# Kernel tuning notes

Measured on AMD Instinct MI355X. Metric: run time of the kernel, lower is better.

The kernel has to match this reference:

```python
import jax, jax.numpy as jnp
import numpy as np

N_E, N_C, N_DL, N_IT, N_EP, N_HA, N_CA, N_AS = 11964, 188, 100, 7, 100, 10, 10, 7
D = 128
B, S = 256, 400
N_V = N_E + 1      # hypergraph vertices (exercises)
N_HE = N_C + 1     # hyperedges (concepts)
MEMB = 3           # concept memberships per exercise
BN_EPS = 1e-5


def _hg_v2v_mean(X, pair_v, pair_e):
    # HGNN+ smoothing: vertex -> hyperedge (mean) -> vertex (mean)
    ones_e = jnp.ones(pair_e.shape, X.dtype)
    e_deg = jnp.clip(jax.ops.segment_sum(ones_e, pair_e, num_segments=N_HE), 1.0)
    v_deg = jnp.clip(jax.ops.segment_sum(ones_e, pair_v, num_segments=N_V), 1.0)
    E = jax.ops.segment_sum(X[pair_v], pair_e, num_segments=N_HE) / e_deg[:, None]
    return jax.ops.segment_sum(E[pair_e], pair_v, num_segments=N_V) / v_deg[:, None]


def _hgnnp_conv(X, W, b, gamma, beta, mean, var, pair_v, pair_e, is_last):
    X = X @ W + b
    X = (X - mean) * jax.lax.rsqrt(var + BN_EPS) * gamma + beta  # eval-mode BN
    X = _hg_v2v_mean(X, pair_v, pair_e)
    if not is_last:
        X = jax.nn.relu(X)
    return X


def setup_inputs() -> dict:
    key = jax.random.key(0)
    ks = jax.random.split(key, 32)
    inp = {}
    inp['input_e'] = jax.random.randint(ks[0], (B, S), 0, N_V)
    inp['input_ed'] = jax.random.randint(ks[1], (B, S), 0, N_DL + 1)
    inp['input_ep'] = jax.random.randint(ks[2], (B, S), 0, N_EP + 1)
    inp['input_a'] = jax.random.randint(ks[3], (B, S), 0, 2)
    inp['input_as'] = jax.random.randint(ks[4], (B, S), 0, N_AS + 1)
    inp['input_ha'] = jax.random.randint(ks[5], (B, S), 0, N_HA + 1)
    inp['input_ca'] = jax.random.randint(ks[6], (B, S), 0, N_CA + 1)
    inp['input_it'] = jax.random.randint(ks[7], (B, S), 0, N_IT + 1)
    inp['deliver_h'] = jnp.zeros((B, D), jnp.float32)
    # hypergraph incidence (exercise-concept Q-matrix edges)
    rng = np.random.default_rng(0)
    inp['pair_v'] = jnp.asarray(np.repeat(np.arange(N_V), MEMB))
    inp['pair_e'] = jnp.asarray(rng.integers(0, N_HE, size=N_V * MEMB))
    inp['ec_map'] = jax.random.randint(ks[8], (N_V,), 0, N_HE)
    inp['ecd_map'] = jax.random.randint(ks[9], (N_V,), 0, N_DL + 1)
    # embedding tables (xavier-ish scale)
    def emb(k, n):
        return jax.random.normal(k, (n, D), jnp.float32) * 0.05
    inp['e_table'] = emb(ks[10], N_V)
    inp['c_table'] = emb(ks[11], N_HE)
    inp['ed_table'] = emb(ks[12], N_DL + 1)
    inp['cd_table'] = emb(ks[13], N_DL + 1)
    inp['a_table'] = emb(ks[14], 2)
    inp['it_table'] = emb(ks[15], N_IT + 1)
    inp['ep_table'] = emb(ks[16], N_EP + 1)
    inp['ha_table'] = emb(ks[17], N_HA + 1)
    inp['ca_table'] = emb(ks[18], N_CA + 1)
    inp['as_table'] = emb(ks[19], N_AS + 1)
    # HGNNP conv 1 & 2
    def lin(k, din, dout):
        return jax.random.normal(k, (din, dout), jnp.float32) * (1.0 / np.sqrt(din))
    inp['W1'] = lin(ks[20], D, D); inp['b1'] = jnp.zeros((D,), jnp.float32)
    inp['g1'] = jnp.ones((D,), jnp.float32); inp['be1'] = jnp.zeros((D,), jnp.float32)
    inp['m1'] = jnp.zeros((D,), jnp.float32); inp['v1'] = jnp.ones((D,), jnp.float32)
    inp['W2'] = lin(ks[21], D, D); inp['b2'] = jnp.zeros((D,), jnp.float32)
    inp['g2'] = jnp.ones((D,), jnp.float32); inp['be2'] = jnp.zeros((D,), jnp.float32)
    inp['m2'] = jnp.zeros((D,), jnp.float32); inp['v2'] = jnp.ones((D,), jnp.float32)
    # linear_i: (d_e + d_dl + d_ep + d_c + d_dl) -> d_x
    inp['Wi'] = lin(ks[22], 5 * D, D); inp['bi'] = jnp.zeros((D,), jnp.float32)
    # GRU knowledge-state cell: input = concat(x, a_emb) -> 2D, hidden D, 3 gates
    inp['Wg'] = lin(ks[23], 2 * D, 3 * D)
    inp['Ug'] = lin(ks[24], D, 3 * D)
    inp['bg'] = jnp.zeros((3 * D,), jnp.float32)
    # linear_predicting_e: d_x -> 1
    inp['We'] = lin(ks[25], D, 1); inp['beo'] = jnp.zeros((1,), jnp.float32)
    # linear_predicting_s: 4*d -> 1
    inp['Ws'] = lin(ks[26], 4 * D, 1); inp['bs'] = jnp.zeros((1,), jnp.float32)
    return inp


def reference(input_e, input_ed, input_ep, input_a, input_as, input_ha, input_ca, input_it,
              deliver_h, pair_v, pair_e, ec_map, ecd_map,
              e_table, c_table, ed_table, cd_table, a_table, it_table, ep_table,
              ha_table, ca_table, as_table,
              W1, b1, g1, be1, m1, v1, W2, b2, g2, be2, m2, v2,
              Wi, bi, Wg, Ug, bg, We, beo, Ws, bs):
    # 2-layer HGNN+ over the exercise hypergraph
    X = _hgnnp_conv(e_table, W1, b1, g1, be1, m1, v1, pair_v, pair_e, is_last=False)
    X = _hgnnp_conv(X, W2, b2, g2, be2, m2, v2, pair_v, pair_e, is_last=True)
    # embedding gathers  [B,S,D]
    e_emb = X[input_e]
    c_emb = c_table[ec_map[input_e]]
    cd_emb = cd_table[ecd_map[input_e]]
    ed_emb = ed_table[input_ed]
    ep_emb = ep_table[input_ep]
    x = jnp.tanh(jnp.concatenate([e_emb, ed_emb, ep_emb, c_emb, cd_emb], -1) @ Wi + bi)  # [B,S,D]
    a_emb = a_table[input_a]
    xs = jnp.moveaxis(jnp.concatenate([x, a_emb], -1), 1, 0)  # [S,B,2D]
    xp = jnp.moveaxis(x, 1, 0)                                # [S,B,D]

    def step(h, inputs):
        xin, xq = inputs
        y = jax.nn.sigmoid((h * xq) @ We + beo)[..., 0]  # predict from prior knowledge state
        gi = xin @ Wg + bg
        gh = h @ Ug
        iz, ir, inn = jnp.split(gi, 3, -1)
        hz, hr, hn = jnp.split(gh, 3, -1)
        z = jax.nn.sigmoid(iz + hz)
        r = jax.nn.sigmoid(ir + hr)
        n = jnp.tanh(inn + r * hn)
        return (1.0 - z) * n + z * h, y

    _, ys = jax.lax.scan(step, deliver_h, (xs, xp))
    pred_main = jnp.moveaxis(ys, 0, 1)  # [B,S]
    s_in = jnp.concatenate([ha_table[input_ha], ca_table[input_ca],
                            as_table[input_as], it_table[input_it]], -1)
    pred_s = jax.nn.sigmoid(s_in @ Ws + bs)[..., 0]  # [B,S]
    return pred_s, pred_main
```

## Files before the change

kernel.cpp:

```cpp
#include <hip/hip_runtime.h>

#define N_V   11965
#define N_HE  189
#define NPAIR 35895
#define BB    256
#define SS    400
#define DD    128
#define BSR   102400

typedef __bf16 bf16x8 __attribute__((ext_vector_type(8)));
typedef float  f32x4  __attribute__((ext_vector_type(4)));

__device__ __forceinline__ ushort f2bf(float f) {
    unsigned x = __float_as_uint(f);
    return (ushort)((x + 0x7FFFu + ((x >> 16) & 1u)) >> 16);
}
__device__ __forceinline__ float bf2f(ushort u) { return __uint_as_float(((unsigned)u) << 16); }
__device__ __forceinline__ float sigm(float x) { return 1.f / (1.f + __expf(-x)); }
__device__ __forceinline__ float tanh_f(float x) { return 2.f * sigm(2.f * x) - 1.f; }
__device__ __forceinline__ float blo(unsigned u) { return __uint_as_float(u << 16); }
__device__ __forceinline__ float bhi(unsigned u) { return __uint_as_float(u); }

struct P1Args {
    const int* pair_e;
    const float *b1, *g1, *be1, *m1, *v1;
    const float *b2, *g2, *be2, *m2, *v2;
    const float *W1, *W2, *Wi, *Wg, *Ug;
    const float *ed_t, *ep_t, *c_t, *cd_t, *a_t, *bi, *bg;
    const float *ha_t, *ca_t, *as_t, *it_t, *Ws;
    int* e_deg;
    float* aff;
    ushort *W1T, *W2T, *WiTe, *WgT, *UgT;
    float *edW, *epW, *cW, *cdW, *agi, *sd;
};

__global__ __launch_bounds__(384) void p1_kernel(P1Args A) {
    int bid = blockIdx.x, t = threadIdx.x;
    if (bid == 0) {
        if (t < 128) {
            float s = A.g1[t] * rsqrtf(A.v1[t] + 1e-5f);
            A.aff[t] = s;
            A.aff[128 + t] = A.b1[t] * s + A.be1[t] - A.m1[t] * s;
        } else if (t < 256) {
            int d = t - 128;
            float s = A.g2[d] * rsqrtf(A.v2[d] + 1e-5f);
            A.aff[256 + d] = s;
            A.aff[384 + d] = A.b2[d] * s + A.be2[d] - A.m2[d] * s;
        }
        return;
    }
    bid -= 1;
    if (bid < 94) {
        int p = bid * 384 + t;
        if (p < NPAIR) atomicAdd(&A.e_deg[A.pair_e[p]], 1);
        return;
    }
    bid -= 94;
    if (bid < 43) {
        int i = bid * 384 + t;
        if (i < 16384) { int k = i >> 7, n = i & 127; A.W1T[n * 128 + k] = f2bf(A.W1[i]); }
        return;
    }
    bid -= 43;
    if (bid < 43) {
        int i = bid * 384 + t;
        if (i < 16384) { int k = i >> 7, n = i & 127; A.W2T[n * 128 + k] = f2bf(A.W2[i]); }
        return;
    }
    bid -= 43;
    if (bid < 43) {
        int i = bid * 384 + t;
        if (i < 16384) { int k = i >> 7, n = i & 127; A.WiTe[n * 128 + k] = f2bf(A.Wi[i]); }
        return;
    }
    bid -= 43;
    if (bid < 128) {
        int i = bid * 384 + t;
        if (i < 49152) { int k = i / 384, n = i % 384; A.WgT[n * 128 + k] = f2bf(A.Wg[i]); }
        return;
    }
    bid -= 128;
    if (bid < 128) {
        int i = bid * 384 + t;
        if (i < 49152) { int k = i / 384, n = i % 384; A.UgT[n * 128 + k] = f2bf(A.Ug[i]); }
        return;
    }
    bid -= 128;
    if (bid < 101) {
        if (t < 128) {
            float acc = 0.f;
            for (int k = 0; k < 128; ++k)
                acc += A.ed_t[bid * 128 + k] * A.Wi[(128 + k) * 128 + t];
            A.edW[bid * 128 + t] = acc + A.bi[t];
        }
        return;
    }
    bid -= 101;
    if (bid < 101) {
        if (t < 128) {
            float acc = 0.f;
            for (int k = 0; k < 128; ++k)
                acc += A.ep_t[bid * 128 + k] * A.Wi[(256 + k) * 128 + t];
            A.epW[bid * 128 + t] = acc;
        }
        return;
    }
    bid -= 101;
    if (bid < 189) {
        if (t < 128) {
            float acc = 0.f;
            for (int k = 0; k < 128; ++k)
                acc += A.c_t[bid * 128 + k] * A.Wi[(384 + k) * 128 + t];
            A.cW[bid * 128 + t] = acc;
        }
        return;
    }
    bid -= 189;
    if (bid < 101) {
        if (t < 128) {
            float acc = 0.f;
            for (int k = 0; k < 128; ++k)
                acc += A.cd_t[bid * 128 + k] * A.Wi[(512 + k) * 128 + t];
            A.cdW[bid * 128 + t] = acc;
        }
        return;
    }
    bid -= 101;
    if (bid < 2) {
        float acc = 0.f;
        for (int k = 0; k < 128; ++k)
            acc += A.a_t[bid * 128 + k] * A.Wg[(128 + k) * 384 + t];
        A.agi[bid * 384 + t] = acc + A.bg[t];
        return;
    }
    bid -= 2;
    {
        int r = bid;
        const float* tab; int woff, row;
        if (r < 11)      { tab = A.ha_t; row = r;      woff = 0;   }
        else if (r < 22) { tab = A.ca_t; row = r - 11; woff = 128; }
        else if (r < 30) { tab = A.as_t; row = r - 22; woff = 256; }
        else             { tab = A.it_t; row = r - 30; woff = 384; }
        if (t < 64) {
            float p = tab[row * 128 + t] * A.Ws[woff + t]
                    + tab[row * 128 + 64 + t] * A.Ws[woff + 64 + t];
            #pragma unroll
            for (int o = 32; o > 0; o >>= 1) p += __shfl_xor(p, o);
            if (t == 0) A.sd[r] = p;
        }
    }
}

__global__ void cvt_kernel(const float* __restrict__ src, ushort* __restrict__ dst, int n) {
    int i = blockIdx.x * 256 + threadIdx.x;
    if (i < n) dst[i] = f2bf(src[i]);
}

__global__ void csr_prefix(const int* __restrict__ e_deg, int* __restrict__ start) {
    __shared__ int sc[256];
    int t = threadIdx.x;
    int d = (t < N_HE) ? e_deg[t] : 0;
    sc[t] = d;
    __syncthreads();
    for (int off = 1; off < 256; off <<= 1) {
        int v = (t >= off) ? sc[t - off] : 0;
        __syncthreads();
        sc[t] += v;
        __syncthreads();
    }
    if (t < N_HE) start[t] = sc[t] - d;
    if (t == N_HE - 1) start[N_HE] = sc[t];
}

__global__ void csr_fill(const int* __restrict__ pair_e, const int* __restrict__ pair_v,
                         const int* __restrict__ start, int* __restrict__ cursor,
                         int* __restrict__ list) {
    int p = blockIdx.x * 384 + threadIdx.x;
    if (p >= NPAIR) return;
    int e = pair_e[p];
    int pos = atomicAdd(&cursor[e], 1);
    list[start[e] + pos] = pair_v[p];
}

template <int NT>
__global__ __launch_bounds__(256) void gemm_mfma(
    const ushort* __restrict__ Amat, const ushort* __restrict__ BT,
    float* __restrict__ out, int M,
    const float* __restrict__ colS, const float* __restrict__ colB,
    const float* __restrict__ agi, const int* __restrict__ aidx) {
    const int N = NT * 16;
    int lane = threadIdx.x & 63, wave = threadIdx.x >> 6;
    int q = lane >> 4, c = lane & 15;
    int rowbase = blockIdx.x * 64 + wave * 16;
    int arow = rowbase + c;
    if (arow > M - 1) arow = M - 1;
    f32x4 acc[NT];
#pragma unroll
    for (int i = 0; i < NT; ++i) acc[i] = (f32x4){0.f, 0.f, 0.f, 0.f};
#pragma unroll
    for (int ko = 0; ko < 4; ++ko) {
        bf16x8 af = *(const bf16x8*)(Amat + (size_t)arow * 128 + ko * 32 + q * 8);
#pragma unroll
        for (int nt = 0; nt < NT; ++nt) {
            bf16x8 bfr = *(const bf16x8*)(BT + (size_t)(nt * 16 + c) * 128 + ko * 32 + q * 8);
            acc[nt] = __builtin_amdgcn_mfma_f32_16x16x32_bf16(af, bfr, acc[nt], 0, 0, 0);
        }
    }
#pragma unroll
    for (int nt = 0; nt < NT; ++nt) {
        int col = nt * 16 + c;
        float s = colS ? colS[col] : 1.f;
        float bb = colB ? colB[col] : 0.f;
#pragma unroll
        for (int r = 0; r < 4; ++r) {
            int row = rowbase + q * 4 + r;
            if (row < M) {
                float v = acc[nt][r] * s + bb;
                if (agi) v += agi[aidx[row] * N + col];
                out[(size_t)row * N + col] = v;
            }
        }
    }
}

__global__ __launch_bounds__(512) void edge_mean(const float* __restrict__ Y,
                                                 const int* __restrict__ list,
                                                 const int* __restrict__ start,
                                                 float* __restrict__ E) {
    __shared__ float red[4][128];
    int e = blockIdx.x;
    int d = threadIdx.x & 127, g = threadIdx.x >> 7;
    int s0 = start[e], n = start[e + 1] - s0;
    float acc = 0.f;
    for (int i = g; i < n; i += 4) acc += Y[(size_t)list[s0 + i] * DD + d];
    red[g][d] = acc;
    __syncthreads();
    if (g == 0) {
        float v = red[0][d] + red[1][d] + red[2][d] + red[3][d];
        E[e * DD + d] = v / (float)(n > 0 ? n : 1);
    }
}

__global__ void v_mean(const float* __restrict__ E, const int* __restrict__ pair_e,
                       ushort* __restrict__ Xo, int relu) {
    int idx = blockIdx.x * 256 + threadIdx.x;
    if (idx >= N_V * DD) return;
    int v = idx >> 7, d = idx & 127;
    float a = E[pair_e[3 * v] * DD + d] + E[pair_e[3 * v + 1] * DD + d] +
              E[pair_e[3 * v + 2] * DD + d];
    a *= (1.f / 3.f);
    if (relu) a = fmaxf(a, 0.f);
    Xo[idx] = f2bf(a);
}

__global__ void k3_kernel(const int* __restrict__ in_e, const int* __restrict__ in_ed,
                          const int* __restrict__ in_ep, const float* __restrict__ XW,
                          const float* __restrict__ cW, const float* __restrict__ cdW,
                          const float* __restrict__ edW, const float* __restrict__ epW,
                          const int* __restrict__ ec_map, const int* __restrict__ ecd_map,
                          ushort* __restrict__ xbf) {
    int idx = blockIdx.x * 256 + threadIdx.x;
    if (idx >= BSR * DD) return;
    int row = idx >> 7, d = idx & 127;
    int e = in_e[row];
    float v = XW[(size_t)e * DD + d] + cW[ec_map[e] * DD + d] + cdW[ecd_map[e] * DD + d] +
              edW[in_ed[row] * DD + d] + epW[in_ep[row] * DD + d];
    xbf[idx] = f2bf(tanh_f(v));
}

__global__ void pred_s_kernel(const int* __restrict__ ha, const int* __restrict__ ca,
                              const int* __restrict__ as_, const int* __restrict__ it,
                              const float* __restrict__ sd, const float* __restrict__ bs,
                              float* __restrict__ out) {
    int i = blockIdx.x * 256 + threadIdx.x;
    if (i >= BSR) return;
    float v = sd[ha[i]] + sd[11 + ca[i]] + sd[22 + as_[i]] + sd[30 + it[i]] + bs[0];
    out[i] = sigm(v);
}

__global__ void
__attribute__((amdgpu_flat_work_group_size(768, 768)))
gru_scan(
    const float* __restrict__ gi, const ushort* __restrict__ xb,
    const ushort* __restrict__ UgT, const float* __restrict__ h0,
    const float* __restrict__ We, const float* __restrict__ beo_p,
    float* __restrict__ out) {
    __shared__ __align__(16) float h_s[128];
    __shared__ float p_s[128];
    __shared__ float pp[4][392];
    int b = blockIdx.x, t = threadIdx.x;
    int kq = t / 192;
    int cp = t % 192;
    const uint4* WA = (const uint4*)(UgT + (size_t)cp * 128 + kq * 32);
    const uint4* WB = (const uint4*)(UgT + (size_t)(cp + 192) * 128 + kq * 32);
    uint4 A0 = WA[0], A1 = WA[1], A2 = WA[2], A3 = WA[3];
    uint4 B0 = WB[0], B1 = WB[1], B2 = WB[2], B3 = WB[3];
    unsigned a0 = A0.x, a1 = A0.y, a2 = A0.z, a3 = A0.w;
    unsigned a4 = A1.x, a5 = A1.y, a6 = A1.z, a7 = A1.w;
    unsigned a8 = A2.x, a9 = A2.y, a10 = A2.z, a11 = A2.w;
    unsigned a12 = A3.x, a13 = A3.y, a14 = A3.z, a15 = A3.w;
    unsigned c0 = B0.x, c1 = B0.y, c2 = B0.z, c3 = B0.w;
    unsigned c4 = B1.x, c5 = B1.y, c6 = B1.z, c7 = B1.w;
    unsigned c8 = B2.x, c9 = B2.y, c10 = B2.z, c11 = B2.w;
    unsigned c12 = B3.x, c13 = B3.y, c14 = B3.z, c15 = B3.w;
    float beo = beo_p[0];
    float wev = 0.f, hreg = 0.f;
    if (t < 128) {
        wev = We[t];
        hreg = h0[b * 128 + t];
        h_s[t] = hreg;
    }
    const float* gip = gi + (size_t)b * SS * 384;
    const ushort* xp = xb + (size_t)b * SS * 128;
    float gz_nx = 0.f, gr_nx = 0.f, gn_nx = 0.f, xw_nx = 0.f;
    if (t < 128) {
        gz_nx = gip[t];
        gr_nx = gip[128 + t];
        gn_nx = gip[256 + t];
        xw_nx = bf2f(xp[t]) * wev;
    }
    float* omain = out + BSR + b * SS;
    __syncthreads();
    for (int s = 0; s < SS; ++s) {
#define PINA(X) asm volatile("" : "+a"(X));
        PINA(a0) PINA(a1) PINA(a2) PINA(a3) PINA(a4) PINA(a5) PINA(a6) PINA(a7)
        PINA(a8) PINA(a9) PINA(a10) PINA(a11) PINA(a12) PINA(a13) PINA(a14) PINA(a15)
        PINA(c0) PINA(c1) PINA(c2) PINA(c3) PINA(c4) PINA(c5) PINA(c6) PINA(c7)
        PINA(c8) PINA(c9) PINA(c10) PINA(c11) PINA(c12) PINA(c13) PINA(c14) PINA(c15)
#undef PINA
        float gz = gz_nx, gr = gr_nx, gn = gn_nx, xw = xw_nx;
        if (s + 1 < SS && t < 128) {
            const float* g2 = gip + (size_t)(s + 1) * 384;
            gz_nx = g2[t];
            gr_nx = g2[128 + t];
            gn_nx = g2[256 + t];
            xw_nx = bf2f(xp[(size_t)(s + 1) * 128 + t]) * wev;
        }
        const float4* h4 = (const float4*)h_s + kq * 8;
        float accA = 0.f, accB = 0.f;
#define FB2(HI, U0, U1, U2, U3, V0, V1, V2, V3) { \
        float4 hv0 = h4[HI], hv1 = h4[HI + 1]; \
        accA = fmaf(hv0.x, blo(U0), accA); accA = fmaf(hv0.y, bhi(U0), accA); \
        accA = fmaf(hv0.z, blo(U1), accA); accA = fmaf(hv0.w, bhi(U1), accA); \
        accA = fmaf(hv1.x, blo(U2), accA); accA = fmaf(hv1.y, bhi(U2), accA); \
        accA = fmaf(hv1.z, blo(U3), accA); accA = fmaf(hv1.w, bhi(U3), accA); \
        accB = fmaf(hv0.x, blo(V0), accB); accB = fmaf(hv0.y, bhi(V0), accB); \
        accB = fmaf(hv0.z, blo(V1), accB); accB = fmaf(hv0.w, bhi(V1), accB); \
        accB = fmaf(hv1.x, blo(V2), accB); accB = fmaf(hv1.y, bhi(V2), accB); \
        accB = fmaf(hv1.z, blo(V3), accB); accB = fmaf(hv1.w, bhi(V3), accB); }
        FB2(0, a0, a1, a2, a3, c0, c1, c2, c3)
        FB2(2, a4, a5, a6, a7, c4, c5, c6, c7)
        FB2(4, a8, a9, a10, a11, c8, c9, c10, c11)
        FB2(6, a12, a13, a14, a15, c12, c13, c14, c15)
#undef FB2
        pp[kq][cp] = accA;
        pp[kq][cp + 192] = accB;
        if (t >= 704 && s > 0) {
            int l = t - 704;
            float pv = p_s[l] + p_s[l + 64];
#pragma unroll
            for (int o = 32; o > 0; o >>= 1) pv += __shfl_xor(pv, o);
            if (l == 0) omain[s - 1] = sigm(pv + beo);
        }
        __syncthreads();
        if (t < 128) {
            float Sz = pp[0][t] + pp[1][t] + pp[2][t] + pp[3][t];
            float Sr = pp[0][128 + t] + pp[1][128 + t] + pp[2][128 + t] + pp[3][128 + t];
            float Sn = pp[0][256 + t] + pp[1][256 + t] + pp[2][256 + t] + pp[3][256 + t];
            float z = sigm(gz + Sz);
            float r = sigm(gr + Sr);
            float n = tanh_f(gn + r * Sn);
            p_s[t] = hreg * xw;
            hreg = (1.f - z) * n + z * hreg;
            h_s[t] = hreg;
        }
        __syncthreads();
    }
    if (t >= 704) {
        int l = t - 704;
        float pv = p_s[l] + p_s[l + 64];
#pragma unroll
        for (int o = 32; o > 0; o >>= 1) pv += __shfl_xor(pv, o);
        if (l == 0) omain[SS - 1] = sigm(pv + beo);
    }
}

extern "C" void kernel_launch(void* const* d_in, const int* in_sizes, int n_in,
                              void* d_out, int out_size, void* d_ws, size_t ws_size,
                              hipStream_t stream) {
    const int* in_e   = (const int*)d_in[0];
    const int* in_ed  = (const int*)d_in[1];
    const int* in_ep  = (const int*)d_in[2];
    const int* in_a   = (const int*)d_in[3];
    const int* in_as  = (const int*)d_in[4];
    const int* in_ha  = (const int*)d_in[5];
    const int* in_ca  = (const int*)d_in[6];
    const int* in_it  = (const int*)d_in[7];
    const float* deliver_h = (const float*)d_in[8];
    const int* pair_v = (const int*)d_in[9];
    const int* pair_e = (const int*)d_in[10];
    const int* ec_map = (const int*)d_in[11];
    const int* ecd_map= (const int*)d_in[12];
    const float* e_table  = (const float*)d_in[13];
    const float* c_table  = (const float*)d_in[14];
    const float* ed_table = (const float*)d_in[15];
    const float* cd_table = (const float*)d_in[16];
    const float* a_table  = (const float*)d_in[17];
    const float* it_table = (const float*)d_in[18];
    const float* ep_table = (const float*)d_in[19];
    const float* ha_table = (const float*)d_in[20];
    const float* ca_table = (const float*)d_in[21];
    const float* as_table = (const float*)d_in[22];
    const float* W1 = (const float*)d_in[23];
    const float* b1 = (const float*)d_in[24];
    const float* g1 = (const float*)d_in[25];
    const float* be1= (const float*)d_in[26];
    const float* m1 = (const float*)d_in[27];
    const float* v1 = (const float*)d_in[28];
    const float* W2 = (const float*)d_in[29];
    const float* b2 = (const float*)d_in[30];
    const float* g2 = (const float*)d_in[31];
    const float* be2= (const float*)d_in[32];
    const float* m2 = (const float*)d_in[33];
    const float* v2 = (const float*)d_in[34];
    const float* Wi = (const float*)d_in[35];
    const float* bi = (const float*)d_in[36];
    const float* Wg = (const float*)d_in[37];
    const float* Ug = (const float*)d_in[38];
    const float* bg = (const float*)d_in[39];
    const float* We = (const float*)d_in[40];
    const float* beo= (const float*)d_in[41];
    const float* Ws = (const float*)d_in[42];
    const float* bs = (const float*)d_in[43];
    float* out = (float*)d_out;
    char* ws = (char*)d_ws;

    size_t off = 0;
    auto alloc = [&](size_t bytes) { size_t o = off; off += (bytes + 255) & ~(size_t)255; return o; };
    size_t o_degcur = alloc(378 * 4);
    size_t o_start  = alloc(190 * 4);
    size_t o_list   = alloc((size_t)NPAIR * 4);
    size_t o_aff    = alloc(512 * 4);
    size_t o_W1T    = alloc(16384 * 2);
    size_t o_W2T    = alloc(16384 * 2);
    size_t o_WiTe   = alloc(16384 * 2);
    size_t o_WgT    = alloc(49152 * 2);
    size_t o_UgT    = alloc(49152 * 2);
    size_t o_edW    = alloc(101 * 128 * 4);
    size_t o_epW    = alloc(101 * 128 * 4);
    size_t o_cW     = alloc(189 * 128 * 4);
    size_t o_cdW    = alloc(101 * 128 * 4);
    size_t o_agi    = alloc(2 * 384 * 4);
    size_t o_sd     = alloc(38 * 4);
    size_t o_etb    = alloc((size_t)N_V * DD * 2);
    size_t o_E      = alloc((size_t)N_HE * DD * 4);
    size_t o_Y      = alloc((size_t)N_V * DD * 4);
    size_t o_X1     = alloc((size_t)N_V * DD * 2);
    size_t o_X2     = alloc((size_t)N_V * DD * 2);
    size_t o_XW     = alloc((size_t)N_V * DD * 4);
    size_t o_xbf    = alloc((size_t)BSR * DD * 2);
    size_t o_gi     = alloc((size_t)BSR * 384 * 4);

    int*    e_deg  = (int*)(ws + o_degcur);
    int*    cursor = e_deg + 189;
    int*    startp = (int*)(ws + o_start);
    int*    listp  = (int*)(ws + o_list);
    float*  aff    = (float*)(ws + o_aff);
    ushort* W1T    = (ushort*)(ws + o_W1T);
    ushort* W2T    = (ushort*)(ws + o_W2T);
    ushort* WiTe   = (ushort*)(ws + o_WiTe);
    ushort* WgT    = (ushort*)(ws + o_WgT);
    ushort* UgTp   = (ushort*)(ws + o_UgT);
    float*  edW    = (float*)(ws + o_edW);
    float*  epW    = (float*)(ws + o_epW);
    float*  cW     = (float*)(ws + o_cW);
    float*  cdW    = (float*)(ws + o_cdW);
    float*  agi    = (float*)(ws + o_agi);
    float*  sd     = (float*)(ws + o_sd);
    ushort* e_tb   = (ushort*)(ws + o_etb);
    float*  E      = (float*)(ws + o_E);
    float*  Y      = (float*)(ws + o_Y);
    ushort* X1b    = (ushort*)(ws + o_X1);
    ushort* X2b    = (ushort*)(ws + o_X2);
    float*  XW     = (float*)(ws + o_XW);
    ushort* xbf    = (ushort*)(ws + o_xbf);
    float*  gi     = (float*)(ws + o_gi);

    hipMemsetAsync(ws + o_degcur, 0, 378 * 4, stream);

    P1Args pa;
    pa.pair_e = pair_e;
    pa.b1 = b1; pa.g1 = g1; pa.be1 = be1; pa.m1 = m1; pa.v1 = v1;
    pa.b2 = b2; pa.g2 = g2; pa.be2 = be2; pa.m2 = m2; pa.v2 = v2;
    pa.W1 = W1; pa.W2 = W2; pa.Wi = Wi; pa.Wg = Wg; pa.Ug = Ug;
    pa.ed_t = ed_table; pa.ep_t = ep_table; pa.c_t = c_table; pa.cd_t = cd_table;
    pa.a_t = a_table; pa.bi = bi; pa.bg = bg;
    pa.ha_t = ha_table; pa.ca_t = ca_table; pa.as_t = as_table; pa.it_t = it_table; pa.Ws = Ws;
    pa.e_deg = e_deg; pa.aff = aff;
    pa.W1T = W1T; pa.W2T = W2T; pa.WiTe = WiTe; pa.WgT = WgT; pa.UgT = UgTp;
    pa.edW = edW; pa.epW = epW; pa.cW = cW; pa.cdW = cdW; pa.agi = agi; pa.sd = sd;
    p1_kernel<<<1012, 384, 0, stream>>>(pa);

    cvt_kernel<<<(N_V * DD + 255) / 256, 256, 0, stream>>>(e_table, e_tb, N_V * DD);
    csr_prefix<<<1, 256, 0, stream>>>(e_deg, startp);
    csr_fill<<<94, 384, 0, stream>>>(pair_e, pair_v, startp, cursor, listp);

    pred_s_kernel<<<(BSR + 255) / 256, 256, 0, stream>>>(in_ha, in_ca, in_as, in_it, sd, bs, out);

    gemm_mfma<8><<<(N_V + 63) / 64, 256, 0, stream>>>(e_tb, W1T, Y, N_V, aff, aff + 128,
                                                      nullptr, nullptr);
    edge_mean<<<N_HE, 512, 0, stream>>>(Y, listp, startp, E);
    v_mean<<<(N_V * DD + 255) / 256, 256, 0, stream>>>(E, pair_e, X1b, 1);
    gemm_mfma<8><<<(N_V + 63) / 64, 256, 0, stream>>>(X1b, W2T, Y, N_V, aff + 256, aff + 384,
                                                      nullptr, nullptr);
    edge_mean<<<N_HE, 512, 0, stream>>>(Y, listp, startp, E);
    v_mean<<<(N_V * DD + 255) / 256, 256, 0, stream>>>(E, pair_e, X2b, 0);
    gemm_mfma<8><<<(N_V + 63) / 64, 256, 0, stream>>>(X2b, WiTe, XW, N_V, nullptr, nullptr,
                                                      nullptr, nullptr);
    k3_kernel<<<(BSR * DD + 255) / 256, 256, 0, stream>>>(in_e, in_ed, in_ep, XW, cW, cdW, edW,
                                                          epW, ec_map, ecd_map, xbf);
    gemm_mfma<24><<<BSR / 64, 256, 0, stream>>>(xbf, WgT, gi, BSR, nullptr, nullptr, agi, in_a);
    gru_scan<<<BB, 768, 0, stream>>>(gi, xbf, UgTp, deliver_h, We, beo, out);
}
```

Baseline: 976.5 us.

## Store GRU input gates in bf16 and keep fp32 recurrent weights with lane broadcasts

```diff
diff --git a/kernel.cpp b/kernel.cpp
--- a/kernel.cpp
+++ b/kernel.cpp
@@ -18,19 +18,17 @@
 __device__ __forceinline__ float bf2f(ushort u) { return __uint_as_float(((unsigned)u) << 16); }
 __device__ __forceinline__ float sigm(float x) { return 1.f / (1.f + __expf(-x)); }
 __device__ __forceinline__ float tanh_f(float x) { return 2.f * sigm(2.f * x) - 1.f; }
-__device__ __forceinline__ float blo(unsigned u) { return __uint_as_float(u << 16); }
-__device__ __forceinline__ float bhi(unsigned u) { return __uint_as_float(u); }
 
 struct P1Args {
     const int* pair_e;
     const float *b1, *g1, *be1, *m1, *v1;
     const float *b2, *g2, *be2, *m2, *v2;
-    const float *W1, *W2, *Wi, *Wg, *Ug;
+    const float *W1, *W2, *Wi, *Wg;
     const float *ed_t, *ep_t, *c_t, *cd_t, *a_t, *bi, *bg;
     const float *ha_t, *ca_t, *as_t, *it_t, *Ws;
     int* e_deg;
     float* aff;
-    ushort *W1T, *W2T, *WiTe, *WgT, *UgT;
+    ushort *W1T, *W2T, *WiTe, *WgT;
     float *edW, *epW, *cW, *cdW, *agi, *sd;
 };
 
@@ -77,12 +75,6 @@
     if (bid < 128) {
         int i = bid * 384 + t;
         if (i < 49152) { int k = i / 384, n = i % 384; A.WgT[n * 128 + k] = f2bf(A.Wg[i]); }
-        return;
-    }
-    bid -= 128;
-    if (bid < 128) {
-        int i = bid * 384 + t;
-        if (i < 49152) { int k = i / 384, n = i % 384; A.UgT[n * 128 + k] = f2bf(A.Ug[i]); }
         return;
     }
     bid -= 128;
@@ -182,10 +174,10 @@
     list[start[e] + pos] = pair_v[p];
 }
 
-template <int NT>
+template <int NT, bool OB>
 __global__ __launch_bounds__(256) void gemm_mfma(
     const ushort* __restrict__ Amat, const ushort* __restrict__ BT,
-    float* __restrict__ out, int M,
+    void* __restrict__ outp, int M,
     const float* __restrict__ colS, const float* __restrict__ colB,
     const float* __restrict__ agi, const int* __restrict__ aidx) {
     const int N = NT * 16;
@@ -217,7 +209,8 @@
             if (row < M) {
                 float v = acc[nt][r] * s + bb;
                 if (agi) v += agi[aidx[row] * N + col];
-                out[(size_t)row * N + col] = v;
+                if (OB) ((ushort*)outp)[(size_t)row * N + col] = f2bf(v);
+                else    ((float*)outp)[(size_t)row * N + col] = v;
             }
         }
     }
@@ -281,8 +274,8 @@
 __global__ void
 __attribute__((amdgpu_flat_work_group_size(768, 768)))
 gru_scan(
-    const float* __restrict__ gi, const ushort* __restrict__ xb,
-    const ushort* __restrict__ UgT, const float* __restrict__ h0,
+    const ushort* __restrict__ gi, const ushort* __restrict__ xb,
+    const float* __restrict__ Ug, const float* __restrict__ h0,
     const float* __restrict__ We, const float* __restrict__ beo_p,
     float* __restrict__ out) {
     __shared__ __align__(16) float h_s[128];
@@ -291,18 +284,19 @@
     int b = blockIdx.x, t = threadIdx.x;
     int kq = t / 192;
     int cp = t % 192;
-    const uint4* WA = (const uint4*)(UgT + (size_t)cp * 128 + kq * 32);
-    const uint4* WB = (const uint4*)(UgT + (size_t)(cp + 192) * 128 + kq * 32);
-    uint4 A0 = WA[0], A1 = WA[1], A2 = WA[2], A3 = WA[3];
-    uint4 B0 = WB[0], B1 = WB[1], B2 = WB[2], B3 = WB[3];
-    unsigned a0 = A0.x, a1 = A0.y, a2 = A0.z, a3 = A0.w;
-    unsigned a4 = A1.x, a5 = A1.y, a6 = A1.z, a7 = A1.w;
-    unsigned a8 = A2.x, a9 = A2.y, a10 = A2.z, a11 = A2.w;
-    unsigned a12 = A3.x, a13 = A3.y, a14 = A3.z, a15 = A3.w;
-    unsigned c0 = B0.x, c1 = B0.y, c2 = B0.z, c3 = B0.w;
-    unsigned c4 = B1.x, c5 = B1.y, c6 = B1.z, c7 = B1.w;
-    unsigned c8 = B2.x, c9 = B2.y, c10 = B2.z, c11 = B2.w;
-    unsigned c12 = B3.x, c13 = B3.y, c14 = B3.z, c15 = B3.w;
+    const float* WAp = Ug + (size_t)(kq * 32) * 384 + cp;
+    const float* WBp = WAp + 192;
+#define LDW4(P, a, b_, c_, d_, J) \
+    float a = P[(J) * 384], b_ = P[(J + 1) * 384], c_ = P[(J + 2) * 384], d_ = P[(J + 3) * 384];
+    LDW4(WAp, A0, A1, A2, A3, 0)     LDW4(WAp, A4, A5, A6, A7, 4)
+    LDW4(WAp, A8, A9, A10, A11, 8)   LDW4(WAp, A12, A13, A14, A15, 12)
+    LDW4(WAp, A16, A17, A18, A19, 16) LDW4(WAp, A20, A21, A22, A23, 20)
+    LDW4(WAp, A24, A25, A26, A27, 24) LDW4(WAp, A28, A29, A30, A31, 28)
+    LDW4(WBp, B0, B1, B2, B3, 0)     LDW4(WBp, B4, B5, B6, B7, 4)
+    LDW4(WBp, B8, B9, B10, B11, 8)   LDW4(WBp, B12, B13, B14, B15, 12)
+    LDW4(WBp, B16, B17, B18, B19, 16) LDW4(WBp, B20, B21, B22, B23, 20)
+    LDW4(WBp, B24, B25, B26, B27, 24) LDW4(WBp, B28, B29, B30, B31, 28)
+#undef LDW4
     float beo = beo_p[0];
     float wev = 0.f, hreg = 0.f;
     if (t < 128) {
@@ -310,49 +304,51 @@
         hreg = h0[b * 128 + t];
         h_s[t] = hreg;
     }
-    const float* gip = gi + (size_t)b * SS * 384;
+    const ushort* gip = gi + (size_t)b * SS * 384;
     const ushort* xp = xb + (size_t)b * SS * 128;
     float gz_nx = 0.f, gr_nx = 0.f, gn_nx = 0.f, xw_nx = 0.f;
     if (t < 128) {
-        gz_nx = gip[t];
-        gr_nx = gip[128 + t];
-        gn_nx = gip[256 + t];
+        gz_nx = bf2f(gip[t]);
+        gr_nx = bf2f(gip[128 + t]);
+        gn_nx = bf2f(gip[256 + t]);
         xw_nx = bf2f(xp[t]) * wev;
     }
+    const float4* hqp = (const float4*)h_s + kq * 8 + (t & 7);
     float* omain = out + BSR + b * SS;
     __syncthreads();
     for (int s = 0; s < SS; ++s) {
 #define PINA(X) asm volatile("" : "+a"(X));
-        PINA(a0) PINA(a1) PINA(a2) PINA(a3) PINA(a4) PINA(a5) PINA(a6) PINA(a7)
-        PINA(a8) PINA(a9) PINA(a10) PINA(a11) PINA(a12) PINA(a13) PINA(a14) PINA(a15)
-        PINA(c0) PINA(c1) PINA(c2) PINA(c3) PINA(c4) PINA(c5) PINA(c6) PINA(c7)
-        PINA(c8) PINA(c9) PINA(c10) PINA(c11) PINA(c12) PINA(c13) PINA(c14) PINA(c15)
+        PINA(A0) PINA(A1) PINA(A2) PINA(A3) PINA(A4) PINA(A5) PINA(A6) PINA(A7)
+        PINA(A8) PINA(A9) PINA(A10) PINA(A11) PINA(A12) PINA(A13) PINA(A14) PINA(A15)
+        PINA(A16) PINA(A17) PINA(A18) PINA(A19) PINA(A20) PINA(A21) PINA(A22) PINA(A23)
+        PINA(A24) PINA(A25) PINA(A26) PINA(A27) PINA(A28) PINA(A29) PINA(A30) PINA(A31)
+        PINA(B0) PINA(B1) PINA(B2) PINA(B3) PINA(B4) PINA(B5) PINA(B6) PINA(B7)
+        PINA(B8) PINA(B9) PINA(B10) PINA(B11) PINA(B12) PINA(B13) PINA(B14) PINA(B15)
+        PINA(B16) PINA(B17) PINA(B18) PINA(B19) PINA(B20) PINA(B21) PINA(B22) PINA(B23)
+        PINA(B24) PINA(B25) PINA(B26) PINA(B27) PINA(B28) PINA(B29) PINA(B30) PINA(B31)
 #undef PINA
         float gz = gz_nx, gr = gr_nx, gn = gn_nx, xw = xw_nx;
         if (s + 1 < SS && t < 128) {
-            const float* g2 = gip + (size_t)(s + 1) * 384;
-            gz_nx = g2[t];
-            gr_nx = g2[128 + t];
-            gn_nx = g2[256 + t];
+            const ushort* g2 = gip + (size_t)(s + 1) * 384;
+            gz_nx = bf2f(g2[t]);
+            gr_nx = bf2f(g2[128 + t]);
+            gn_nx = bf2f(g2[256 + t]);
             xw_nx = bf2f(xp[(size_t)(s + 1) * 128 + t]) * wev;
         }
-        const float4* h4 = (const float4*)h_s + kq * 8;
+        float4 hv = *hqp;
         float accA = 0.f, accB = 0.f;
-#define FB2(HI, U0, U1, U2, U3, V0, V1, V2, V3) { \
-        float4 hv0 = h4[HI], hv1 = h4[HI + 1]; \
-        accA = fmaf(hv0.x, blo(U0), accA); accA = fmaf(hv0.y, bhi(U0), accA); \
-        accA = fmaf(hv0.z, blo(U1), accA); accA = fmaf(hv0.w, bhi(U1), accA); \
-        accA = fmaf(hv1.x, blo(U2), accA); accA = fmaf(hv1.y, bhi(U2), accA); \
-        accA = fmaf(hv1.z, blo(U3), accA); accA = fmaf(hv1.w, bhi(U3), accA); \
-        accB = fmaf(hv0.x, blo(V0), accB); accB = fmaf(hv0.y, bhi(V0), accB); \
-        accB = fmaf(hv0.z, blo(V1), accB); accB = fmaf(hv0.w, bhi(V1), accB); \
-        accB = fmaf(hv1.x, blo(V2), accB); accB = fmaf(hv1.y, bhi(V2), accB); \
-        accB = fmaf(hv1.z, blo(V3), accB); accB = fmaf(hv1.w, bhi(V3), accB); }
-        FB2(0, a0, a1, a2, a3, c0, c1, c2, c3)
-        FB2(2, a4, a5, a6, a7, c4, c5, c6, c7)
-        FB2(4, a8, a9, a10, a11, c8, c9, c10, c11)
-        FB2(6, a12, a13, a14, a15, c12, c13, c14, c15)
-#undef FB2
+#define STEPK(L, C, WA_, WB_) { \
+        float hk = __int_as_float(__builtin_amdgcn_readlane(__float_as_int(hv.C), L)); \
+        accA = fmaf(hk, WA_, accA); accB = fmaf(hk, WB_, accB); }
+        STEPK(0, x, A0, B0)   STEPK(0, y, A1, B1)   STEPK(0, z, A2, B2)   STEPK(0, w, A3, B3)
+        STEPK(1, x, A4, B4)   STEPK(1, y, A5, B5)   STEPK(1, z, A6, B6)   STEPK(1, w, A7, B7)
+        STEPK(2, x, A8, B8)   STEPK(2, y, A9, B9)   STEPK(2, z, A10, B10) STEPK(2, w, A11, B11)
+        STEPK(3, x, A12, B12) STEPK(3, y, A13, B13) STEPK(3, z, A14, B14) STEPK(3, w, A15, B15)
+        STEPK(4, x, A16, B16) STEPK(4, y, A17, B17) STEPK(4, z, A18, B18) STEPK(4, w, A19, B19)
+        STEPK(5, x, A20, B20) STEPK(5, y, A21, B21) STEPK(5, z, A22, B22) STEPK(5, w, A23, B23)
+        STEPK(6, x, A24, B24) STEPK(6, y, A25, B25) STEPK(6, z, A26, B26) STEPK(6, w, A27, B27)
+        STEPK(7, x, A28, B28) STEPK(7, y, A29, B29) STEPK(7, z, A30, B30) STEPK(7, w, A31, B31)
+#undef STEPK
         pp[kq][cp] = accA;
         pp[kq][cp + 192] = accB;
         if (t >= 704 && s > 0) {
@@ -445,7 +441,6 @@
     size_t o_W2T    = alloc(16384 * 2);
     size_t o_WiTe   = alloc(16384 * 2);
     size_t o_WgT    = alloc(49152 * 2);
-    size_t o_UgT    = alloc(49152 * 2);
     size_t o_edW    = alloc(101 * 128 * 4);
     size_t o_epW    = alloc(101 * 128 * 4);
     size_t o_cW     = alloc(189 * 128 * 4);
@@ -459,7 +454,7 @@
     size_t o_X2     = alloc((size_t)N_V * DD * 2);
     size_t o_XW     = alloc((size_t)N_V * DD * 4);
     size_t o_xbf    = alloc((size_t)BSR * DD * 2);
-    size_t o_gi     = alloc((size_t)BSR * 384 * 4);
+    size_t o_gi     = alloc((size_t)BSR * 384 * 2);
 
     int*    e_deg  = (int*)(ws + o_degcur);
     int*    cursor = e_deg + 189;
@@ -470,7 +465,6 @@
     ushort* W2T    = (ushort*)(ws + o_W2T);
     ushort* WiTe   = (ushort*)(ws + o_WiTe);
     ushort* WgT    = (ushort*)(ws + o_WgT);
-    ushort* UgTp   = (ushort*)(ws + o_UgT);
     float*  edW    = (float*)(ws + o_edW);
     float*  epW    = (float*)(ws + o_epW);
     float*  cW     = (float*)(ws + o_cW);
@@ -484,7 +478,7 @@
     ushort* X2b    = (ushort*)(ws + o_X2);
     float*  XW     = (float*)(ws + o_XW);
     ushort* xbf    = (ushort*)(ws + o_xbf);
-    float*  gi     = (float*)(ws + o_gi);
+    ushort* gi     = (ushort*)(ws + o_gi);
 
     hipMemsetAsync(ws + o_degcur, 0, 378 * 4, stream);
 
@@ -492,14 +486,14 @@
     pa.pair_e = pair_e;
     pa.b1 = b1; pa.g1 = g1; pa.be1 = be1; pa.m1 = m1; pa.v1 = v1;
     pa.b2 = b2; pa.g2 = g2; pa.be2 = be2; pa.m2 = m2; pa.v2 = v2;
-    pa.W1 = W1; pa.W2 = W2; pa.Wi = Wi; pa.Wg = Wg; pa.Ug = Ug;
+    pa.W1 = W1; pa.W2 = W2; pa.Wi = Wi; pa.Wg = Wg;
     pa.ed_t = ed_table; pa.ep_t = ep_table; pa.c_t = c_table; pa.cd_t = cd_table;
     pa.a_t = a_table; pa.bi = bi; pa.bg = bg;
     pa.ha_t = ha_table; pa.ca_t = ca_table; pa.as_t = as_table; pa.it_t = it_table; pa.Ws = Ws;
     pa.e_deg = e_deg; pa.aff = aff;
-    pa.W1T = W1T; pa.W2T = W2T; pa.WiTe = WiTe; pa.WgT = WgT; pa.UgT = UgTp;
+    pa.W1T = W1T; pa.W2T = W2T; pa.WiTe = WiTe; pa.WgT = WgT;
     pa.edW = edW; pa.epW = epW; pa.cW = cW; pa.cdW = cdW; pa.agi = agi; pa.sd = sd;
-    p1_kernel<<<1012, 384, 0, stream>>>(pa);
+    p1_kernel<<<884, 384, 0, stream>>>(pa);
 
     cvt_kernel<<<(N_V * DD + 255) / 256, 256, 0, stream>>>(e_table, e_tb, N_V * DD);
     csr_prefix<<<1, 256, 0, stream>>>(e_deg, startp);
@@ -507,18 +501,19 @@
 
     pred_s_kernel<<<(BSR + 255) / 256, 256, 0, stream>>>(in_ha, in_ca, in_as, in_it, sd, bs, out);
 
-    gemm_mfma<8><<<(N_V + 63) / 64, 256, 0, stream>>>(e_tb, W1T, Y, N_V, aff, aff + 128,
-                                                      nullptr, nullptr);
+    gemm_mfma<8, false><<<(N_V + 63) / 64, 256, 0, stream>>>(e_tb, W1T, Y, N_V, aff, aff + 128,
+                                                             nullptr, nullptr);
     edge_mean<<<N_HE, 512, 0, stream>>>(Y, listp, startp, E);
     v_mean<<<(N_V * DD + 255) / 256, 256, 0, stream>>>(E, pair_e, X1b, 1);
-    gemm_mfma<8><<<(N_V + 63) / 64, 256, 0, stream>>>(X1b, W2T, Y, N_V, aff + 256, aff + 384,
-                                                      nullptr, nullptr);
+    gemm_mfma<8, false><<<(N_V + 63) / 64, 256, 0, stream>>>(X1b, W2T, Y, N_V, aff + 256,
+                                                             aff + 384, nullptr, nullptr);
     edge_mean<<<N_HE, 512, 0, stream>>>(Y, listp, startp, E);
     v_mean<<<(N_V * DD + 255) / 256, 256, 0, stream>>>(E, pair_e, X2b, 0);
-    gemm_mfma<8><<<(N_V + 63) / 64, 256, 0, stream>>>(X2b, WiTe, XW, N_V, nullptr, nullptr,
-                                                      nullptr, nullptr);
+    gemm_mfma<8, false><<<(N_V + 63) / 64, 256, 0, stream>>>(X2b, WiTe, XW, N_V, nullptr,
+                                                             nullptr, nullptr, nullptr);
     k3_kernel<<<(BSR * DD + 255) / 256, 256, 0, stream>>>(in_e, in_ed, in_ep, XW, cW, cdW, edW,
                                                           epW, ec_map, ecd_map, xbf);
-    gemm_mfma<24><<<BSR / 64, 256, 0, stream>>>(xbf, WgT, gi, BSR, nullptr, nullptr, agi, in_a);
-    gru_scan<<<BB, 768, 0, stream>>>(gi, xbf, UgTp, deliver_h, We, beo, out);
-}
+    gemm_mfma<24, true><<<BSR / 64, 256, 0, stream>>>(xbf, WgT, gi, BSR, nullptr, nullptr,
+                                                      agi, in_a);
+    gru_scan<<<BB, 768, 0, stream>>>(gi, xbf, Ug, deliver_h, We, beo, out);
+}
```

After: 1.103 ms. +12.9%, slower.
